# Kernel optimization log

Measured on AMD Instinct MI355X. Metric: run time of the kernel, lower is better.

Reference implementation:

```python
import jax, jax.numpy as jnp
import numpy as np

N, E, D, L = 50000, 800000, 128, 2
EPS = 1e-7

def _logmap0(y):
    # Poincare ball (c=1) logmap at origin: artanh(||y||) * y / ||y||
    n = jnp.linalg.norm(y, axis=-1, keepdims=True)
    nc = jnp.clip(n, EPS, 1.0 - 1e-5)
    return jnp.arctanh(nc) * y / jnp.maximum(n, EPS)

def _expmap0(u):
    # Poincare ball (c=1) expmap at origin: tanh(||u||) * u / ||u||
    n = jnp.linalg.norm(u, axis=-1, keepdims=True)
    return jnp.tanh(n) * u / jnp.maximum(n, EPS)

def _l2norm(x):
    # F.normalize(p=2, dim=1)
    return x / jnp.maximum(jnp.linalg.norm(x, axis=1, keepdims=True), 1e-12)

def setup_inputs() -> dict:
    key = jax.random.key(0)
    ks = jax.random.split(key, 12)
    src = jax.random.randint(ks[0], (E,), 0, N)
    dst = jax.random.randint(ks[1], (E,), 0, N)
    e_emb = jax.random.normal(ks[2], (N, D), jnp.float32)
    b_emb = jax.random.normal(ks[3], (N, D), jnp.float32) * 0.1  # inside Poincare ball
    s_emb = jax.random.normal(ks[4], (N, D), jnp.float32)
    sc = 0.05
    eW = jax.random.normal(ks[5], (L, D, D), jnp.float32) * sc
    eB = jax.random.normal(ks[6], (L, D), jnp.float32) * sc
    bW = jax.random.normal(ks[7], (L, D, D), jnp.float32) * sc
    bB = jax.random.normal(ks[8], (L, D), jnp.float32) * sc
    sW = jax.random.normal(ks[9], (L, D, D), jnp.float32) * sc
    sB = jax.random.normal(ks[10], (L, D), jnp.float32) * sc
    return dict(e_emb=e_emb, b_emb=b_emb, s_emb=s_emb, eW=eW, eB=eB,
                bW=bW, bB=bB, sW=sW, sB=sB, src=src, dst=dst)

def reference(e_emb, b_emb, s_emb, eW, eB, bW, bB, sW, sB, src, dst):
    n_nodes = e_emb.shape[0]
    ones_e = jnp.ones(src.shape[0], jnp.float32)
    in_deg = jax.ops.segment_sum(ones_e, dst, num_segments=n_nodes)
    out_deg = jax.ops.segment_sum(ones_e, src, num_segments=n_nodes)
    # DGL GraphConv norm='both': D_out^{-1/2} (sum over in-neighbors) D_in^{-1/2}
    norm_out = jnp.where(out_deg > 0, out_deg ** -0.5, 0.0)[:, None]
    norm_in = jnp.where(in_deg > 0, in_deg ** -0.5, 0.0)[:, None]
    inv_in = jnp.where(in_deg > 0, 1.0 / in_deg, 0.0)[:, None]  # mean reduce

    def agg_sum(h):
        return jax.ops.segment_sum(h[src], dst, num_segments=n_nodes)

    for l in range(L):
        # Euclidean branch: GraphConv(norm='both') then LeakyReLU(0.2)
        h = agg_sum(e_emb * norm_out) * norm_in
        e_emb = jax.nn.leaky_relu(h @ eW[l].T + eB[l], negative_slope=0.2)
        # Hyperbolic branch: logmap0 -> Linear -> neighbor mean -> expmap0
        tan_b = _logmap0(b_emb) @ bW[l].T + bB[l]
        b_emb = _expmap0(agg_sum(tan_b) * inv_in)
        # Spherical branch: normalize -> Linear -> neighbor mean -> normalize
        tan_s = _l2norm(s_emb) @ sW[l].T + sB[l]
        s_emb = _l2norm(agg_sum(tan_s) * inv_in)
    return (e_emb, b_emb, s_emb)
```

## Files before the change

kernel.cpp:

```cpp
#include <hip/hip_runtime.h>
#include <math.h>

#define DD 128
#define PSTRIDE 384

typedef _Float16 half8 __attribute__((ext_vector_type(8)));
typedef _Float16 half2v __attribute__((ext_vector_type(2)));
typedef float floatx4 __attribute__((ext_vector_type(4)));

__device__ __forceinline__ float wave_sum_f(float x) {
#pragma unroll
  for (int m = 32; m >= 1; m >>= 1) x += __shfl_xor(x, m, 64);
  return x;
}
__device__ __forceinline__ int wave_sum_i(int x) {
#pragma unroll
  for (int m = 32; m >= 1; m >>= 1) x += __shfl_xor(x, m, 64);
  return x;
}

__global__ void degrees_kernel(const int* __restrict__ src, const int* __restrict__ dst,
                               int* __restrict__ out_deg, int* __restrict__ in_deg, int E) {
  int e = blockIdx.x * blockDim.x + threadIdx.x;
  if (e < E) {
    atomicAdd(&out_deg[src[e]], 1);
    atomicAdd(&in_deg[dst[e]], 1);
  }
}

__global__ void norms_kernel(const int* __restrict__ in_deg, const int* __restrict__ out_deg,
                             float* __restrict__ norm_in, float* __restrict__ norm_out,
                             float* __restrict__ inv_in, int N) {
  int i = blockIdx.x * blockDim.x + threadIdx.x;
  if (i < N) {
    int di = in_deg[i], dq = out_deg[i];
    norm_in[i]  = di > 0 ? 1.0f / sqrtf((float)di) : 0.0f;
    norm_out[i] = dq > 0 ? 1.0f / sqrtf((float)dq) : 0.0f;
    inv_in[i]   = di > 0 ? 1.0f / (float)di : 0.0f;
  }
}

__global__ void part_sum_kernel(const int* __restrict__ deg, int* __restrict__ part, int N) {
  __shared__ int wsum[4];
  int t = threadIdx.x, lane = t & 63, w = t >> 6;
  int i = blockIdx.x * 256 + t;
  int x = (i < N) ? deg[i] : 0;
  int s = wave_sum_i(x);
  if (lane == 0) wsum[w] = s;
  __syncthreads();
  if (t == 0) part[blockIdx.x] = wsum[0] + wsum[1] + wsum[2] + wsum[3];
}

__global__ void part_scan_kernel(int* __restrict__ part, int nb) {
  __shared__ int wsum[4];
  int t = threadIdx.x, lane = t & 63, w = t >> 6;
  int x = (t < nb) ? part[t] : 0;
  int v = x;
#pragma unroll
  for (int off = 1; off < 64; off <<= 1) {
    int y = __shfl_up(v, off, 64);
    if (lane >= off) v += y;
  }
  if (lane == 63) wsum[w] = v;
  __syncthreads();
  int base = 0;
  for (int q = 0; q < w; ++q) base += wsum[q];
  if (t < nb) part[t] = base + v - x;
}

__global__ void local_scan_kernel(const int* __restrict__ deg, const int* __restrict__ part,
                                  int* __restrict__ row_off, int N, int E) {
  __shared__ int wsum[4];
  int t = threadIdx.x, lane = t & 63, w = t >> 6;
  int i = blockIdx.x * 256 + t;
  int x = (i < N) ? deg[i] : 0;
  int v = x;
#pragma unroll
  for (int off = 1; off < 64; off <<= 1) {
    int y = __shfl_up(v, off, 64);
    if (lane >= off) v += y;
  }
  if (lane == 63) wsum[w] = v;
  __syncthreads();
  int base = 0;
  for (int q = 0; q < w; ++q) base += wsum[q];
  if (i < N) row_off[i] = part[blockIdx.x] + base + v - x;
  if (blockIdx.x == 0 && t == 0) row_off[N] = E;
}

__global__ void csr_fill_kernel(const int* __restrict__ src, const int* __restrict__ dst,
                                const int* __restrict__ row_off, int* __restrict__ cursor,
                                int* __restrict__ csr_src, int E) {
  int e = blockIdx.x * blockDim.x + threadIdx.x;
  if (e < E) {
    int d = dst[e];
    int pos = row_off[d] + atomicAdd(&cursor[d], 1);
    csr_src[pos] = src[e];
  }
}

template <int MODE>
__global__ void scale_kernel(const float* __restrict__ x, float* __restrict__ s, int N) {
  int lane = threadIdx.x & 63;
  int v = blockIdx.x * 4 + (threadIdx.x >> 6);
  if (v >= N) return;
  float2 a = ((const float2*)x)[(size_t)v * 64 + lane];
  float n = sqrtf(wave_sum_f(a.x * a.x + a.y * a.y));
  float f;
  if (MODE == 1) {
    float nc = fminf(fmaxf(n, 1e-7f), 1.0f - 1e-5f);
    f = atanhf(nc) / fmaxf(n, 1e-7f);
  } else {
    f = 1.0f / fmaxf(n, 1e-12f);
  }
  if (lane == 0) s[v] = f;
}

__global__ void wcvt_kernel(const float* __restrict__ Wf, _Float16* __restrict__ Wh, int n) {
  int i = blockIdx.x * 256 + threadIdx.x;
  if (i < n) Wh[i] = (_Float16)Wf[i];
}

__global__ void pack_half_kernel(const float* __restrict__ x, _Float16* __restrict__ Pp, int N) {
  int i = blockIdx.x * 256 + threadIdx.x;
  if (i < N * 64) {
    int v = i >> 6, l = i & 63;
    float2 a = ((const float2*)x)[i];
    half2v h; h.x = (_Float16)a.x; h.y = (_Float16)a.y;
    *(half2v*)&Pp[(size_t)v * PSTRIDE + l * 2] = h;
  }
}

template <int MODE>
__global__ __launch_bounds__(256) void gemm_mfma_kernel(const _Float16* __restrict__ Ain,
                                                        const _Float16* __restrict__ Wh,
                                                        const float* __restrict__ Bb,
                                                        const float* __restrict__ scale,
                                                        _Float16* __restrict__ Qout,
                                                        int N) {
  __shared__ _Float16 As[64 * 136];
  __shared__ _Float16 Ws[128 * 136];
  int t = threadIdx.x;
  int rbase = blockIdx.x * 64;

#pragma unroll
  for (int i = 0; i < 8; ++i) {
    int idx = i * 256 + t;
    int row = idx >> 4, col = (idx & 15) * 8;
    *(half8*)&Ws[row * 136 + col] = *(const half8*)&Wh[idx * 8];
  }
  {
    int ar = t >> 2, aseg = t & 3;
    int av = rbase + ar; if (av >= N) av = N - 1;
    const _Float16* Ap = Ain + (size_t)av * PSTRIDE + aseg * 32;
    _Float16* Ad = &As[ar * 136 + aseg * 32];
    *(half8*)&Ad[0]  = *(const half8*)&Ap[0];
    *(half8*)&Ad[8]  = *(const half8*)&Ap[8];
    *(half8*)&Ad[16] = *(const half8*)&Ap[16];
    *(half8*)&Ad[24] = *(const half8*)&Ap[24];
  }
  __syncthreads();

  int lane = t & 63, w = t >> 6;
  int m = lane & 15, quad = lane >> 4;
  int c0 = w * 32;

  half8 bf[2][4];
#pragma unroll
  for (int tj = 0; tj < 2; ++tj)
#pragma unroll
    for (int kk = 0; kk < 4; ++kk)
      bf[tj][kk] = *(const half8*)&Ws[(c0 + tj * 16 + m) * 136 + kk * 32 + quad * 8];

  float bias0 = 0.f, bias1 = 0.f;
  if (MODE) { bias0 = Bb[c0 + m]; bias1 = Bb[c0 + 16 + m]; }

#pragma unroll
  for (int r = 0; r < 4; ++r) {
    int row0 = r * 16;
    floatx4 acc0 = {0.f, 0.f, 0.f, 0.f}, acc1 = {0.f, 0.f, 0.f, 0.f};
#pragma unroll
    for (int kk = 0; kk < 4; ++kk) {
      half8 af = *(const half8*)&As[(row0 + m) * 136 + kk * 32 + quad * 8];
      acc0 = __builtin_amdgcn_mfma_f32_16x16x32_f16(af, bf[0][kk], acc0, 0, 0, 0);
      acc1 = __builtin_amdgcn_mfma_f32_16x16x32_f16(af, bf[1][kk], acc1, 0, 0, 0);
    }
    int vrow = rbase + row0 + quad * 4;
#pragma unroll
    for (int reg = 0; reg < 4; ++reg) {
      int v = vrow + reg;
      if (v < N) {
        float x0 = acc0[reg], x1 = acc1[reg];
        if (MODE) { float s = scale[v]; x0 = x0 * s + bias0; x1 = x1 * s + bias1; }
        Qout[(size_t)v * PSTRIDE + c0 + m]      = (_Float16)x0;
        Qout[(size_t)v * PSTRIDE + c0 + 16 + m] = (_Float16)x1;
      }
    }
  }
}

__global__ void agg_fused_kernel(const _Float16* __restrict__ Q, const int* __restrict__ row_off,
                                 const int* __restrict__ csr_src, const float* __restrict__ norm_out,
                                 const float* __restrict__ norm_in, const float* __restrict__ inv_in,
                                 const float* __restrict__ eBias,
                                 float* __restrict__ oe, float* __restrict__ ob,
                                 float* __restrict__ os, _Float16* __restrict__ Pnext,
                                 float* __restrict__ sb, float* __restrict__ ss,
                                 int N, int write_pack) {
  int lane = threadIdx.x & 63;
  int v = blockIdx.x * 4 + (threadIdx.x >> 6);
  if (v >= N) return;
  const half2v* Ph = (const half2v*)Q;
  int beg = row_off[v], end = row_off[v + 1];
  float ex = 0.f, ey = 0.f, bx = 0.f, by = 0.f, sx = 0.f, sy = 0.f;
  int i = beg;
  for (; i + 4 <= end; i += 4) {
    int n0 = csr_src[i], n1 = csr_src[i + 1], n2 = csr_src[i + 2], n3 = csr_src[i + 3];
    size_t r0 = (size_t)n0 * 192 + lane, r1 = (size_t)n1 * 192 + lane;
    size_t r2 = (size_t)n2 * 192 + lane, r3 = (size_t)n3 * 192 + lane;
    half2v e0 = Ph[r0], e1 = Ph[r1], e2 = Ph[r2], e3 = Ph[r3];
    half2v b0 = Ph[r0 + 64], b1 = Ph[r1 + 64], b2 = Ph[r2 + 64], b3 = Ph[r3 + 64];
    half2v s0 = Ph[r0 + 128], s1 = Ph[r1 + 128], s2 = Ph[r2 + 128], s3 = Ph[r3 + 128];
    float w0 = norm_out[n0], w1 = norm_out[n1], w2 = norm_out[n2], w3 = norm_out[n3];
    ex += (float)e0.x * w0 + (float)e1.x * w1 + (float)e2.x * w2 + (float)e3.x * w3;
    ey += (float)e0.y * w0 + (float)e1.y * w1 + (float)e2.y * w2 + (float)e3.y * w3;
    bx += (float)b0.x + (float)b1.x + (float)b2.x + (float)b3.x;
    by += (float)b0.y + (float)b1.y + (float)b2.y + (float)b3.y;
    sx += (float)s0.x + (float)s1.x + (float)s2.x + (float)s3.x;
    sy += (float)s0.y + (float)s1.y + (float)s2.y + (float)s3.y;
  }
  for (; i < end; ++i) {
    int n0 = csr_src[i];
    size_t r0 = (size_t)n0 * 192 + lane;
    half2v e0 = Ph[r0], b0 = Ph[r0 + 64], s0 = Ph[r0 + 128];
    float w0 = norm_out[n0];
    ex += (float)e0.x * w0; ey += (float)e0.y * w0;
    bx += (float)b0.x; by += (float)b0.y;
    sx += (float)s0.x; sy += (float)s0.y;
  }
  float ni = norm_in[v];
  float2 eb = ((const float2*)eBias)[lane];
  float h0 = ex * ni + eb.x, h1 = ey * ni + eb.y;
  h0 = h0 > 0.f ? h0 : 0.2f * h0;
  h1 = h1 > 0.f ? h1 : 0.2f * h1;
  ((float2*)oe)[(size_t)v * 64 + lane] = make_float2(h0, h1);
  float iv = inv_in[v];
  float ubx = bx * iv, uby = by * iv;
  float usx = sx * iv, usy = sy * iv;
  float nb = sqrtf(wave_sum_f(ubx * ubx + uby * uby));
  float ns = sqrtf(wave_sum_f(usx * usx + usy * usy));
  float fb = tanhf(nb) / fmaxf(nb, 1e-7f);
  float fs = 1.0f / fmaxf(ns, 1e-12f);
  float ob0 = ubx * fb, ob1 = uby * fb;
  float os0 = usx * fs, os1 = usy * fs;
  ((float2*)ob)[(size_t)v * 64 + lane] = make_float2(ob0, ob1);
  ((float2*)os)[(size_t)v * 64 + lane] = make_float2(os0, os1);
  if (write_pack) {
    _Float16* Pr = Pnext + (size_t)v * PSTRIDE + lane * 2;
    half2v he; he.x = (_Float16)h0;  he.y = (_Float16)h1;
    half2v hb; hb.x = (_Float16)ob0; hb.y = (_Float16)ob1;
    half2v hs; hs.x = (_Float16)os0; hs.y = (_Float16)os1;
    *(half2v*)&Pr[0]   = he;
    *(half2v*)&Pr[128] = hb;
    *(half2v*)&Pr[256] = hs;
  }
  if (lane == 0) {
    float mb = fb * nb;
    float ncb = fminf(fmaxf(mb, 1e-7f), 1.0f - 1e-5f);
    sb[v] = atanhf(ncb) / fmaxf(mb, 1e-7f);
    float ms = fs * ns;
    ss[v] = 1.0f / fmaxf(ms, 1e-12f);
  }
}

extern "C" void kernel_launch(void* const* d_in, const int* in_sizes, int n_in,
                              void* d_out, int out_size, void* d_ws, size_t ws_size,
                              hipStream_t stream) {
  const float* e0 = (const float*)d_in[0];
  const float* b0 = (const float*)d_in[1];
  const float* s0 = (const float*)d_in[2];
  const float* eW = (const float*)d_in[3];
  const float* eB = (const float*)d_in[4];
  const float* bW = (const float*)d_in[5];
  const float* bB = (const float*)d_in[6];
  const float* sW = (const float*)d_in[7];
  const float* sB = (const float*)d_in[8];
  const int* src = (const int*)d_in[9];
  const int* dst = (const int*)d_in[10];
  int N = in_sizes[0] / DD;
  int E = in_sizes[9];
  int L = in_sizes[3] / (DD * DD);

  char* w = (char*)d_ws;
  int* in_deg  = (int*)w; w += (size_t)N * 4;
  int* out_deg = (int*)w; w += (size_t)N * 4;
  int* cursor  = (int*)w; w += (size_t)N * 4;
  int* row_off = (int*)w; w += (size_t)(N + 4) * 4;
  int* part    = (int*)w; w += (size_t)1024 * 4;
  int* csr_src = (int*)w; w += (size_t)E * 4;
  float* norm_in  = (float*)w; w += (size_t)N * 4;
  float* norm_out = (float*)w; w += (size_t)N * 4;
  float* inv_in   = (float*)w; w += (size_t)N * 4;
  float* sb       = (float*)w; w += (size_t)N * 4;
  float* ss       = (float*)w; w += (size_t)N * 4;
  _Float16* P     = (_Float16*)w; w += (size_t)N * PSTRIDE * 2;
  _Float16* Q     = (_Float16*)w; w += (size_t)N * PSTRIDE * 2;
  _Float16* whE   = (_Float16*)w; w += (size_t)L * DD * DD * 2;
  _Float16* whB   = (_Float16*)w; w += (size_t)L * DD * DD * 2;
  _Float16* whS   = (_Float16*)w; w += (size_t)L * DD * DD * 2;

  float* oe = (float*)d_out;
  float* ob = oe + (size_t)N * DD;
  float* os = ob + (size_t)N * DD;

  int PB = (N + 255) / 256;
  int AB = (N + 3) / 4;
  int GB = (N + 63) / 64;
  int KB = (N * 64 + 255) / 256;
  int WB = (L * DD * DD + 255) / 256;

  hipMemsetAsync(d_ws, 0, (size_t)3 * N * 4, stream);
  degrees_kernel<<<(E + 255) / 256, 256, 0, stream>>>(src, dst, out_deg, in_deg, E);
  norms_kernel<<<(N + 255) / 256, 256, 0, stream>>>(in_deg, out_deg, norm_in, norm_out, inv_in, N);
  part_sum_kernel<<<PB, 256, 0, stream>>>(in_deg, part, N);
  part_scan_kernel<<<1, 256, 0, stream>>>(part, PB);
  local_scan_kernel<<<PB, 256, 0, stream>>>(in_deg, part, row_off, N, E);
  csr_fill_kernel<<<(E + 255) / 256, 256, 0, stream>>>(src, dst, row_off, cursor, csr_src, E);
  scale_kernel<1><<<AB, 256, 0, stream>>>(b0, sb, N);
  scale_kernel<2><<<AB, 256, 0, stream>>>(s0, ss, N);
  wcvt_kernel<<<WB, 256, 0, stream>>>(eW, whE, L * DD * DD);
  wcvt_kernel<<<WB, 256, 0, stream>>>(bW, whB, L * DD * DD);
  wcvt_kernel<<<WB, 256, 0, stream>>>(sW, whS, L * DD * DD);
  pack_half_kernel<<<KB, 256, 0, stream>>>(e0, P, N);
  pack_half_kernel<<<KB, 256, 0, stream>>>(b0, P + 128, N);
  pack_half_kernel<<<KB, 256, 0, stream>>>(s0, P + 256, N);

  for (int l = 0; l < L; ++l) {
    gemm_mfma_kernel<0><<<GB, 256, 0, stream>>>(P, whE + (size_t)l * DD * DD, nullptr, nullptr, Q, N);
    gemm_mfma_kernel<1><<<GB, 256, 0, stream>>>(P + 128, whB + (size_t)l * DD * DD, bB + (size_t)l * DD, sb, Q + 128, N);
    gemm_mfma_kernel<1><<<GB, 256, 0, stream>>>(P + 256, whS + (size_t)l * DD * DD, sB + (size_t)l * DD, ss, Q + 256, N);
    agg_fused_kernel<<<AB, 256, 0, stream>>>(Q, row_off, csr_src, norm_out, norm_in, inv_in,
                                             eB + (size_t)l * DD, oe, ob, os, P, sb, ss, N,
                                             (l < L - 1) ? 1 : 0);
  }
}
```

Before: 591.7 us.

## Restructure aggregation to 16-lane edge groups with packed edge weights and fused launches

The aggregation kernel now gives each wave four groups of 16 lanes, each handling a different edge with 16-byte half8 loads, and combines the groups with cross-lane shuffles. The CSR now stores (src, norm_out) pairs, so the per-edge norm_out gather goes away. Final fp32 outputs are written only on the last layer, while the packed fp16 buffer and scales are written only when another layer follows. The three GEMMs run as one launch over a 2D grid, and the init conversions and scale computations are merged into fewer kernels. The cost is higher register pressure from 24 accumulators per lane and a CSR twice as large.

```diff
diff --git a/kernel.cpp b/kernel.cpp
--- a/kernel.cpp
+++ b/kernel.cpp
@@ -11,6 +11,11 @@
 __device__ __forceinline__ float wave_sum_f(float x) {
 #pragma unroll
   for (int m = 32; m >= 1; m >>= 1) x += __shfl_xor(x, m, 64);
+  return x;
+}
+__device__ __forceinline__ float g16_sum(float x) {
+#pragma unroll
+  for (int m = 8; m >= 1; m >>= 1) x += __shfl_xor(x, m, 64);
   return x;
 }
 __device__ __forceinline__ int wave_sum_i(int x) {
@@ -64,7 +69,7 @@
   if (lane == 63) wsum[w] = v;
   __syncthreads();
   int base = 0;
-  for (int q = 0; q < w; ++q) base += wsum[q];
+  for (int j = 0; j < w; ++j) base += wsum[j];
   if (t < nb) part[t] = base + v - x;
 }
 
@@ -83,63 +88,76 @@
   if (lane == 63) wsum[w] = v;
   __syncthreads();
   int base = 0;
-  for (int q = 0; q < w; ++q) base += wsum[q];
+  for (int j = 0; j < w; ++j) base += wsum[j];
   if (i < N) row_off[i] = part[blockIdx.x] + base + v - x;
   if (blockIdx.x == 0 && t == 0) row_off[N] = E;
 }
 
 __global__ void csr_fill_kernel(const int* __restrict__ src, const int* __restrict__ dst,
+                                const float* __restrict__ norm_out,
                                 const int* __restrict__ row_off, int* __restrict__ cursor,
-                                int* __restrict__ csr_src, int E) {
+                                int2* __restrict__ csr_sw, int E) {
   int e = blockIdx.x * blockDim.x + threadIdx.x;
   if (e < E) {
-    int d = dst[e];
+    int d = dst[e], s = src[e];
     int pos = row_off[d] + atomicAdd(&cursor[d], 1);
-    csr_src[pos] = src[e];
-  }
-}
-
-template <int MODE>
-__global__ void scale_kernel(const float* __restrict__ x, float* __restrict__ s, int N) {
+    csr_sw[pos] = make_int2(s, __float_as_int(norm_out[s]));
+  }
+}
+
+__global__ void wcvt3_kernel(const float* __restrict__ a, const float* __restrict__ b,
+                             const float* __restrict__ c, _Float16* __restrict__ o, int n) {
+  int i = blockIdx.x * 256 + threadIdx.x;
+  if (i < n) {
+    o[i]         = (_Float16)a[i];
+    o[i + n]     = (_Float16)b[i];
+    o[i + 2 * n] = (_Float16)c[i];
+  }
+}
+
+__global__ void pack_init_kernel(const float* __restrict__ e0, const float* __restrict__ b0,
+                                 const float* __restrict__ s0, _Float16* __restrict__ P,
+                                 float* __restrict__ sb, float* __restrict__ ss, int N) {
   int lane = threadIdx.x & 63;
   int v = blockIdx.x * 4 + (threadIdx.x >> 6);
   if (v >= N) return;
-  float2 a = ((const float2*)x)[(size_t)v * 64 + lane];
-  float n = sqrtf(wave_sum_f(a.x * a.x + a.y * a.y));
-  float f;
-  if (MODE == 1) {
-    float nc = fminf(fmaxf(n, 1e-7f), 1.0f - 1e-5f);
-    f = atanhf(nc) / fmaxf(n, 1e-7f);
-  } else {
-    f = 1.0f / fmaxf(n, 1e-12f);
-  }
-  if (lane == 0) s[v] = f;
-}
-
-__global__ void wcvt_kernel(const float* __restrict__ Wf, _Float16* __restrict__ Wh, int n) {
-  int i = blockIdx.x * 256 + threadIdx.x;
-  if (i < n) Wh[i] = (_Float16)Wf[i];
-}
-
-__global__ void pack_half_kernel(const float* __restrict__ x, _Float16* __restrict__ Pp, int N) {
-  int i = blockIdx.x * 256 + threadIdx.x;
-  if (i < N * 64) {
-    int v = i >> 6, l = i & 63;
-    float2 a = ((const float2*)x)[i];
-    half2v h; h.x = (_Float16)a.x; h.y = (_Float16)a.y;
-    *(half2v*)&Pp[(size_t)v * PSTRIDE + l * 2] = h;
-  }
-}
-
-template <int MODE>
-__global__ __launch_bounds__(256) void gemm_mfma_kernel(const _Float16* __restrict__ Ain,
-                                                        const _Float16* __restrict__ Wh,
-                                                        const float* __restrict__ Bb,
-                                                        const float* __restrict__ scale,
-                                                        _Float16* __restrict__ Qout,
-                                                        int N) {
+  size_t ri = (size_t)v * 64 + lane;
+  float2 e2 = ((const float2*)e0)[ri];
+  float2 b2 = ((const float2*)b0)[ri];
+  float2 s2 = ((const float2*)s0)[ri];
+  _Float16* Pr = P + (size_t)v * PSTRIDE + lane * 2;
+  half2v he; he.x = (_Float16)e2.x; he.y = (_Float16)e2.y;
+  half2v hb; hb.x = (_Float16)b2.x; hb.y = (_Float16)b2.y;
+  half2v hs; hs.x = (_Float16)s2.x; hs.y = (_Float16)s2.y;
+  *(half2v*)&Pr[0]   = he;
+  *(half2v*)&Pr[128] = hb;
+  *(half2v*)&Pr[256] = hs;
+  float nb = sqrtf(wave_sum_f(b2.x * b2.x + b2.y * b2.y));
+  float ns = sqrtf(wave_sum_f(s2.x * s2.x + s2.y * s2.y));
+  if (lane == 0) {
+    float ncb = fminf(fmaxf(nb, 1e-7f), 1.0f - 1e-5f);
+    sb[v] = atanhf(ncb) / fmaxf(nb, 1e-7f);
+    ss[v] = 1.0f / fmaxf(ns, 1e-12f);
+  }
+}
+
+__global__ __launch_bounds__(256) void gemm3_kernel(const _Float16* __restrict__ P,
+                                                    const _Float16* __restrict__ WhE,
+                                                    const _Float16* __restrict__ WhB,
+                                                    const _Float16* __restrict__ WhS,
+                                                    const float* __restrict__ bBl,
+                                                    const float* __restrict__ sBl,
+                                                    const float* __restrict__ sbv,
+                                                    const float* __restrict__ ssv,
+                                                    _Float16* __restrict__ Qout, int N) {
   __shared__ _Float16 As[64 * 136];
   __shared__ _Float16 Ws[128 * 136];
+  int part = blockIdx.y;
+  const _Float16* Ain = P + part * DD;
+  const _Float16* Wh = (part == 0) ? WhE : (part == 1 ? WhB : WhS);
+  const float* Bb = (part == 1) ? bBl : sBl;
+  const float* scv = (part == 1) ? sbv : ssv;
+  _Float16* Qo = Qout + part * DD;
   int t = threadIdx.x;
   int rbase = blockIdx.x * 64;
 
@@ -173,7 +191,7 @@
       bf[tj][kk] = *(const half8*)&Ws[(c0 + tj * 16 + m) * 136 + kk * 32 + quad * 8];
 
   float bias0 = 0.f, bias1 = 0.f;
-  if (MODE) { bias0 = Bb[c0 + m]; bias1 = Bb[c0 + 16 + m]; }
+  if (part) { bias0 = Bb[c0 + m]; bias1 = Bb[c0 + 16 + m]; }
 
 #pragma unroll
   for (int r = 0; r < 4; ++r) {
@@ -191,85 +209,145 @@
       int v = vrow + reg;
       if (v < N) {
         float x0 = acc0[reg], x1 = acc1[reg];
-        if (MODE) { float s = scale[v]; x0 = x0 * s + bias0; x1 = x1 * s + bias1; }
-        Qout[(size_t)v * PSTRIDE + c0 + m]      = (_Float16)x0;
-        Qout[(size_t)v * PSTRIDE + c0 + 16 + m] = (_Float16)x1;
+        if (part) { float s = scv[v]; x0 = x0 * s + bias0; x1 = x1 * s + bias1; }
+        Qo[(size_t)v * PSTRIDE + c0 + m]      = (_Float16)x0;
+        Qo[(size_t)v * PSTRIDE + c0 + 16 + m] = (_Float16)x1;
       }
     }
   }
 }
 
-__global__ void agg_fused_kernel(const _Float16* __restrict__ Q, const int* __restrict__ row_off,
-                                 const int* __restrict__ csr_src, const float* __restrict__ norm_out,
-                                 const float* __restrict__ norm_in, const float* __restrict__ inv_in,
-                                 const float* __restrict__ eBias,
-                                 float* __restrict__ oe, float* __restrict__ ob,
-                                 float* __restrict__ os, _Float16* __restrict__ Pnext,
-                                 float* __restrict__ sb, float* __restrict__ ss,
-                                 int N, int write_pack) {
+__global__ __launch_bounds__(256) void agg_fused_kernel(
+    const _Float16* __restrict__ Q, const int* __restrict__ row_off,
+    const int2* __restrict__ csr_sw, const float* __restrict__ norm_in,
+    const float* __restrict__ inv_in, const float* __restrict__ eBias,
+    float* __restrict__ oe, float* __restrict__ ob, float* __restrict__ os,
+    _Float16* __restrict__ Pnext, float* __restrict__ sb, float* __restrict__ ss,
+    int N, int write_pack, int write_out) {
   int lane = threadIdx.x & 63;
   int v = blockIdx.x * 4 + (threadIdx.x >> 6);
   if (v >= N) return;
-  const half2v* Ph = (const half2v*)Q;
+  int g = lane >> 4, q = lane & 15;
   int beg = row_off[v], end = row_off[v + 1];
-  float ex = 0.f, ey = 0.f, bx = 0.f, by = 0.f, sx = 0.f, sy = 0.f;
+  float eacc[8], bacc[8], sacc[8];
+#pragma unroll
+  for (int j = 0; j < 8; ++j) { eacc[j] = 0.f; bacc[j] = 0.f; sacc[j] = 0.f; }
   int i = beg;
-  for (; i + 4 <= end; i += 4) {
-    int n0 = csr_src[i], n1 = csr_src[i + 1], n2 = csr_src[i + 2], n3 = csr_src[i + 3];
-    size_t r0 = (size_t)n0 * 192 + lane, r1 = (size_t)n1 * 192 + lane;
-    size_t r2 = (size_t)n2 * 192 + lane, r3 = (size_t)n3 * 192 + lane;
-    half2v e0 = Ph[r0], e1 = Ph[r1], e2 = Ph[r2], e3 = Ph[r3];
-    half2v b0 = Ph[r0 + 64], b1 = Ph[r1 + 64], b2 = Ph[r2 + 64], b3 = Ph[r3 + 64];
-    half2v s0 = Ph[r0 + 128], s1 = Ph[r1 + 128], s2 = Ph[r2 + 128], s3 = Ph[r3 + 128];
-    float w0 = norm_out[n0], w1 = norm_out[n1], w2 = norm_out[n2], w3 = norm_out[n3];
-    ex += (float)e0.x * w0 + (float)e1.x * w1 + (float)e2.x * w2 + (float)e3.x * w3;
-    ey += (float)e0.y * w0 + (float)e1.y * w1 + (float)e2.y * w2 + (float)e3.y * w3;
-    bx += (float)b0.x + (float)b1.x + (float)b2.x + (float)b3.x;
-    by += (float)b0.y + (float)b1.y + (float)b2.y + (float)b3.y;
-    sx += (float)s0.x + (float)s1.x + (float)s2.x + (float)s3.x;
-    sy += (float)s0.y + (float)s1.y + (float)s2.y + (float)s3.y;
-  }
-  for (; i < end; ++i) {
-    int n0 = csr_src[i];
-    size_t r0 = (size_t)n0 * 192 + lane;
-    half2v e0 = Ph[r0], b0 = Ph[r0 + 64], s0 = Ph[r0 + 128];
-    float w0 = norm_out[n0];
-    ex += (float)e0.x * w0; ey += (float)e0.y * w0;
-    bx += (float)b0.x; by += (float)b0.y;
-    sx += (float)s0.x; sy += (float)s0.y;
-  }
-  float ni = norm_in[v];
-  float2 eb = ((const float2*)eBias)[lane];
-  float h0 = ex * ni + eb.x, h1 = ey * ni + eb.y;
-  h0 = h0 > 0.f ? h0 : 0.2f * h0;
-  h1 = h1 > 0.f ? h1 : 0.2f * h1;
-  ((float2*)oe)[(size_t)v * 64 + lane] = make_float2(h0, h1);
-  float iv = inv_in[v];
-  float ubx = bx * iv, uby = by * iv;
-  float usx = sx * iv, usy = sy * iv;
-  float nb = sqrtf(wave_sum_f(ubx * ubx + uby * uby));
-  float ns = sqrtf(wave_sum_f(usx * usx + usy * usy));
+  for (; i + 8 <= end; i += 8) {
+    int2 swa = csr_sw[i + g];
+    int2 swb = csr_sw[i + 4 + g];
+    float wa = __int_as_float(swa.y), wb = __int_as_float(swb.y);
+    const _Float16* ra = Q + (size_t)swa.x * PSTRIDE + q * 8;
+    const _Float16* rb = Q + (size_t)swb.x * PSTRIDE + q * 8;
+    half8 ea = *(const half8*)ra;
+    half8 e2 = *(const half8*)rb;
+    half8 ba = *(const half8*)(ra + 128);
+    half8 b2 = *(const half8*)(rb + 128);
+    half8 sa = *(const half8*)(ra + 256);
+    half8 s2 = *(const half8*)(rb + 256);
+#pragma unroll
+    for (int j = 0; j < 8; ++j) {
+      eacc[j] += wa * (float)ea[j];
+      eacc[j] += wb * (float)e2[j];
+      bacc[j] += (float)ba[j];
+      bacc[j] += (float)b2[j];
+      sacc[j] += (float)sa[j];
+      sacc[j] += (float)s2[j];
+    }
+  }
+  if (i + 4 <= end) {
+    int2 sw = csr_sw[i + g];
+    float wgt = __int_as_float(sw.y);
+    const _Float16* rp = Q + (size_t)sw.x * PSTRIDE + q * 8;
+    half8 ev = *(const half8*)rp;
+    half8 bv = *(const half8*)(rp + 128);
+    half8 sv = *(const half8*)(rp + 256);
+#pragma unroll
+    for (int j = 0; j < 8; ++j) {
+      eacc[j] += wgt * (float)ev[j];
+      bacc[j] += (float)bv[j];
+      sacc[j] += (float)sv[j];
+    }
+    i += 4;
+  }
+  if (i + g < end) {
+    int2 sw = csr_sw[i + g];
+    float wgt = __int_as_float(sw.y);
+    const _Float16* rp = Q + (size_t)sw.x * PSTRIDE + q * 8;
+    half8 ev = *(const half8*)rp;
+    half8 bv = *(const half8*)(rp + 128);
+    half8 sv = *(const half8*)(rp + 256);
+#pragma unroll
+    for (int j = 0; j < 8; ++j) {
+      eacc[j] += wgt * (float)ev[j];
+      bacc[j] += (float)bv[j];
+      sacc[j] += (float)sv[j];
+    }
+  }
+#pragma unroll
+  for (int j = 0; j < 8; ++j) {
+    eacc[j] += __shfl_xor(eacc[j], 16, 64);
+    eacc[j] += __shfl_xor(eacc[j], 32, 64);
+    bacc[j] += __shfl_xor(bacc[j], 16, 64);
+    bacc[j] += __shfl_xor(bacc[j], 32, 64);
+    sacc[j] += __shfl_xor(sacc[j], 16, 64);
+    sacc[j] += __shfl_xor(sacc[j], 32, 64);
+  }
+  float ni = norm_in[v], iv = inv_in[v];
+  const float4* ebp = (const float4*)eBias;
+  float4 eb0 = ebp[q * 2], eb1 = ebp[q * 2 + 1];
+  float bias[8] = {eb0.x, eb0.y, eb0.z, eb0.w, eb1.x, eb1.y, eb1.z, eb1.w};
+  float h[8], obv[8], osv[8];
+  float bs2 = 0.f, ss2 = 0.f;
+#pragma unroll
+  for (int j = 0; j < 8; ++j) {
+    float t = eacc[j] * ni + bias[j];
+    h[j] = t > 0.f ? t : 0.2f * t;
+    float ub = bacc[j] * iv; obv[j] = ub; bs2 += ub * ub;
+    float us = sacc[j] * iv; osv[j] = us; ss2 += us * us;
+  }
+  float nb = sqrtf(g16_sum(bs2));
+  float ns = sqrtf(g16_sum(ss2));
   float fb = tanhf(nb) / fmaxf(nb, 1e-7f);
   float fs = 1.0f / fmaxf(ns, 1e-12f);
-  float ob0 = ubx * fb, ob1 = uby * fb;
-  float os0 = usx * fs, os1 = usy * fs;
-  ((float2*)ob)[(size_t)v * 64 + lane] = make_float2(ob0, ob1);
-  ((float2*)os)[(size_t)v * 64 + lane] = make_float2(os0, os1);
+#pragma unroll
+  for (int j = 0; j < 8; ++j) { obv[j] *= fb; osv[j] *= fs; }
+  if (write_out) {
+    if (g == 0) {
+      float4* p = (float4*)(oe + (size_t)v * DD);
+      p[q * 2]     = make_float4(h[0], h[1], h[2], h[3]);
+      p[q * 2 + 1] = make_float4(h[4], h[5], h[6], h[7]);
+    } else if (g == 1) {
+      float4* p = (float4*)(ob + (size_t)v * DD);
+      p[q * 2]     = make_float4(obv[0], obv[1], obv[2], obv[3]);
+      p[q * 2 + 1] = make_float4(obv[4], obv[5], obv[6], obv[7]);
+    } else if (g == 2) {
+      float4* p = (float4*)(os + (size_t)v * DD);
+      p[q * 2]     = make_float4(osv[0], osv[1], osv[2], osv[3]);
+      p[q * 2 + 1] = make_float4(osv[4], osv[5], osv[6], osv[7]);
+    }
+  }
   if (write_pack) {
-    _Float16* Pr = Pnext + (size_t)v * PSTRIDE + lane * 2;
-    half2v he; he.x = (_Float16)h0;  he.y = (_Float16)h1;
-    half2v hb; hb.x = (_Float16)ob0; hb.y = (_Float16)ob1;
-    half2v hs; hs.x = (_Float16)os0; hs.y = (_Float16)os1;
-    *(half2v*)&Pr[0]   = he;
-    *(half2v*)&Pr[128] = hb;
-    *(half2v*)&Pr[256] = hs;
-  }
-  if (lane == 0) {
-    float mb = fb * nb;
-    float ncb = fminf(fmaxf(mb, 1e-7f), 1.0f - 1e-5f);
-    sb[v] = atanhf(ncb) / fmaxf(mb, 1e-7f);
-    float ms = fs * ns;
-    ss[v] = 1.0f / fmaxf(ms, 1e-12f);
+    if (g == 3) {
+      half8 he, hb, hs;
+#pragma unroll
+      for (int j = 0; j < 8; ++j) {
+        he[j] = (_Float16)h[j];
+        hb[j] = (_Float16)obv[j];
+        hs[j] = (_Float16)osv[j];
+      }
+      _Float16* Pr = Pnext + (size_t)v * PSTRIDE + q * 8;
+      *(half8*)&Pr[0]   = he;
+      *(half8*)&Pr[128] = hb;
+      *(half8*)&Pr[256] = hs;
+    }
+    if (lane == 0) {
+      float mb = fb * nb;
+      float ncb = fminf(fmaxf(mb, 1e-7f), 1.0f - 1e-5f);
+      sb[v] = atanhf(ncb) / fmaxf(mb, 1e-7f);
+      float ms = fs * ns;
+      ss[v] = 1.0f / fmaxf(ms, 1e-12f);
+    }
   }
 }
 
@@ -290,14 +368,15 @@
   int N = in_sizes[0] / DD;
   int E = in_sizes[9];
   int L = in_sizes[3] / (DD * DD);
+  int LDD2 = L * DD * DD;
 
   char* w = (char*)d_ws;
   int* in_deg  = (int*)w; w += (size_t)N * 4;
   int* out_deg = (int*)w; w += (size_t)N * 4;
   int* cursor  = (int*)w; w += (size_t)N * 4;
   int* row_off = (int*)w; w += (size_t)(N + 4) * 4;
-  int* part    = (int*)w; w += (size_t)1024 * 4;
-  int* csr_src = (int*)w; w += (size_t)E * 4;
+  int* pscan   = (int*)w; w += (size_t)1024 * 4;
+  int2* csr_sw = (int2*)w; w += (size_t)E * 8;
   float* norm_in  = (float*)w; w += (size_t)N * 4;
   float* norm_out = (float*)w; w += (size_t)N * 4;
   float* inv_in   = (float*)w; w += (size_t)N * 4;
@@ -305,9 +384,9 @@
   float* ss       = (float*)w; w += (size_t)N * 4;
   _Float16* P     = (_Float16*)w; w += (size_t)N * PSTRIDE * 2;
   _Float16* Q     = (_Float16*)w; w += (size_t)N * PSTRIDE * 2;
-  _Float16* whE   = (_Float16*)w; w += (size_t)L * DD * DD * 2;
-  _Float16* whB   = (_Float16*)w; w += (size_t)L * DD * DD * 2;
-  _Float16* whS   = (_Float16*)w; w += (size_t)L * DD * DD * 2;
+  _Float16* whE   = (_Float16*)w; w += (size_t)LDD2 * 2;
+  _Float16* whB   = (_Float16*)w; w += (size_t)LDD2 * 2;
+  _Float16* whS   = (_Float16*)w; w += (size_t)LDD2 * 2;
 
   float* oe = (float*)d_out;
   float* ob = oe + (size_t)N * DD;
@@ -316,31 +395,24 @@
   int PB = (N + 255) / 256;
   int AB = (N + 3) / 4;
   int GB = (N + 63) / 64;
-  int KB = (N * 64 + 255) / 256;
-  int WB = (L * DD * DD + 255) / 256;
 
   hipMemsetAsync(d_ws, 0, (size_t)3 * N * 4, stream);
   degrees_kernel<<<(E + 255) / 256, 256, 0, stream>>>(src, dst, out_deg, in_deg, E);
   norms_kernel<<<(N + 255) / 256, 256, 0, stream>>>(in_deg, out_deg, norm_in, norm_out, inv_in, N);
-  part_sum_kernel<<<PB, 256, 0, stream>>>(in_deg, part, N);
-  part_scan_kernel<<<1, 256, 0, stream>>>(part, PB);
-  local_scan_kernel<<<PB, 256, 0, stream>>>(in_deg, part, row_off, N, E);
-  csr_fill_kernel<<<(E + 255) / 256, 256, 0, stream>>>(src, dst, row_off, cursor, csr_src, E);
-  scale_kernel<1><<<AB, 256, 0, stream>>>(b0, sb, N);
-  scale_kernel<2><<<AB, 256, 0, stream>>>(s0, ss, N);
-  wcvt_kernel<<<WB, 256, 0, stream>>>(eW, whE, L * DD * DD);
-  wcvt_kernel<<<WB, 256, 0, stream>>>(bW, whB, L * DD * DD);
-  wcvt_kernel<<<WB, 256, 0, stream>>>(sW, whS, L * DD * DD);
-  pack_half_kernel<<<KB, 256, 0, stream>>>(e0, P, N);
-  pack_half_kernel<<<KB, 256, 0, stream>>>(b0, P + 128, N);
-  pack_half_kernel<<<KB, 256, 0, stream>>>(s0, P + 256, N);
+  part_sum_kernel<<<PB, 256, 0, stream>>>(in_deg, pscan, N);
+  part_scan_kernel<<<1, 256, 0, stream>>>(pscan, PB);
+  local_scan_kernel<<<PB, 256, 0, stream>>>(in_deg, pscan, row_off, N, E);
+  csr_fill_kernel<<<(E + 255) / 256, 256, 0, stream>>>(src, dst, norm_out, row_off, cursor, csr_sw, E);
+  wcvt3_kernel<<<(LDD2 + 255) / 256, 256, 0, stream>>>(eW, bW, sW, whE, LDD2);
+  pack_init_kernel<<<AB, 256, 0, stream>>>(e0, b0, s0, P, sb, ss, N);
 
   for (int l = 0; l < L; ++l) {
-    gemm_mfma_kernel<0><<<GB, 256, 0, stream>>>(P, whE + (size_t)l * DD * DD, nullptr, nullptr, Q, N);
-    gemm_mfma_kernel<1><<<GB, 256, 0, stream>>>(P + 128, whB + (size_t)l * DD * DD, bB + (size_t)l * DD, sb, Q + 128, N);
-    gemm_mfma_kernel<1><<<GB, 256, 0, stream>>>(P + 256, whS + (size_t)l * DD * DD, sB + (size_t)l * DD, ss, Q + 256, N);
-    agg_fused_kernel<<<AB, 256, 0, stream>>>(Q, row_off, csr_src, norm_out, norm_in, inv_in,
+    size_t lo = (size_t)l * DD * DD;
+    gemm3_kernel<<<dim3(GB, 3), 256, 0, stream>>>(P, whE + lo, whB + lo, whS + lo,
+                                                  bB + (size_t)l * DD, sB + (size_t)l * DD,
+                                                  sb, ss, Q, N);
+    agg_fused_kernel<<<AB, 256, 0, stream>>>(Q, row_off, csr_sw, norm_in, inv_in,
                                              eB + (size_t)l * DD, oe, ob, os, P, sb, ss, N,
-                                             (l < L - 1) ? 1 : 0);
-  }
-}
+                                             (l < L - 1) ? 1 : 0, (l == L - 1) ? 1 : 0);
+  }
+}
```

Result: faster. 523.9 us (-11.5%).
